# Performance work log

Measured on AMD Instinct MI355X. Metric: run time of the kernel, lower is better.

Reference implementation:

```python
import jax, jax.numpy as jnp
import numpy as np

B, S, D, H = 4, 1024, 1024, 16
DK = D // H
N_REL = 5


def setup_inputs() -> dict:
    key = jax.random.key(0)
    ks = jax.random.split(key, 16)
    p = lambda k, shape: (jax.random.normal(k, shape, dtype=jnp.float32) * 0.02)
    return {
        "x": jax.random.normal(ks[0], (B, S, D), dtype=jnp.float32),
        "relation_matrix": jax.random.randint(ks[1], (S, S), 0, N_REL, dtype=jnp.int32),
        "mask": jax.random.randint(ks[2], (B, 1, S, S), 0, 2, dtype=jnp.int32),
        "Wq": p(ks[3], (D, D)), "bq": p(ks[4], (D,)),
        "Wk": p(ks[5], (D, D)), "bk": p(ks[6], (D,)),
        "Wv": p(ks[7], (D, D)), "bv": p(ks[8], (D,)),
        "Wo": p(ks[9], (D, D)), "bo": p(ks[10], (D,)),
        "rel_table": p(ks[11], (N_REL, DK)),
        "gamma": jnp.ones((D,), dtype=jnp.float32),
        "beta": jnp.zeros((D,), dtype=jnp.float32),
    }


def reference(x, relation_matrix, mask, Wq, bq, Wk, bk, Wv, bv, Wo, bo, rel_table, gamma, beta):
    b, s = x.shape[0], x.shape[1]
    residual = x
    # projections -> [B, H, S, DK]
    def proj(W, bias):
        return (x @ W + bias).reshape(b, s, H, DK).transpose(0, 2, 1, 3)
    Q, K, V = proj(Wq, bq), proj(Wk, bk), proj(Wv, bv)
    scores = jnp.einsum('bhid,bhjd->bhij', Q, K) / jnp.sqrt(jnp.float32(DK))
    # relation-embedding additive bias: gather [S,S,DK] then contract with Q
    rel_emb = rel_table[relation_matrix]               # [S, S, DK]
    rel_scores = jnp.einsum('bhid,ijd->bhij', Q, rel_emb)
    scores = scores + rel_scores * 0.5
    scores = jnp.where(mask == 0, jnp.float32(-1e9), scores)
    attention = jax.nn.softmax(scores, axis=-1)
    context = jnp.einsum('bhij,bhjd->bhid', attention, V)
    context = context.transpose(0, 2, 1, 3).reshape(b, s, D)
    output = context @ Wo + bo
    # layer norm (eps = 1e-5, torch default)
    y = output + residual
    mu = jnp.mean(y, axis=-1, keepdims=True)
    var = jnp.mean(jnp.square(y - mu), axis=-1, keepdims=True)
    return (y - mu) * jax.lax.rsqrt(var + 1e-5) * gamma + beta
```

## Files before the change

kernel.cpp:

```cpp
#include <hip/hip_runtime.h>
#include <hip/hip_bf16.h>

typedef unsigned short u16;
typedef unsigned int u32;
typedef unsigned char u8;
typedef __attribute__((ext_vector_type(8))) short short8;
typedef __attribute__((ext_vector_type(4))) float f32x4;

__device__ __forceinline__ float b2f(u16 u) {
    union { float f; u32 i; } z; z.i = ((u32)u) << 16; return z.f;
}
__device__ __forceinline__ u16 f2b(float f) {
    union { float f; u32 i; } z; z.f = f;
    u32 i = z.i;
    u32 r = (i + 0x7FFFu + ((i >> 16) & 1u)) >> 16;
    return (u16)r;
}
__device__ __forceinline__ float ldf(const void* p, size_t i, int f) {
    return f ? ((const float*)p)[i] : b2f(((const u16*)p)[i]);
}
__device__ __forceinline__ void gload_lds16(const void* g, void* l) {
    __builtin_amdgcn_global_load_lds(
        (const __attribute__((address_space(1))) u32*)g,
        (__attribute__((address_space(3))) u32*)l,
        16, 0, 0);
}

struct P14 { const void* p[14]; };
struct S14 { int s[14]; };

__global__ __launch_bounds__(256) void classify(P14 ptrs, S14 szs, int* cls)
{
    __shared__ int   wsm[4], wzr[4], wag[4], way[4], wjk[4];
    __shared__ float wme[4], wmo[4];
    __shared__ int small_[14], zero_[14], gone_[14], junk_[14];
    __shared__ float maxe_[14], maxo_[14];
    int t = threadIdx.x, lane = t & 63, w = t >> 6;
    for (int i = 0; i < 14; ++i) {
        const u16* p16 = (const u16*)ptrs.p[i];
        const u32* p32 = (const u32*)ptrs.p[i];
        int n = szs.s[i];
        int n16 = n < 4096 ? n : 4096;
        int n32 = n16 >> 1;
        int small = 1, zero = 1, allg = 1, anyg = 0, junk = 0;
        float maxe = 0.f, maxo = 0.f;
        for (int k = t; k < n32; k += 256) if (p32[k] >= 8u) small = 0;
        for (int k = t; k < n16; k += 256) {
            u16 ww = p16[k];
            if (ww != 0) zero = 0;
            if (ww == 0x3F80u) anyg = 1;
            else if (ww != 0) allg = 0;
            float a = fabsf(b2f(ww));
            if (k & 1) { if (a < 1e30f && a > maxo) maxo = a; }
            else { if (!(a < 100.0f)) junk++; else if (a > maxe) maxe = a; }
        }
#pragma unroll
        for (int s = 1; s < 64; s <<= 1) {
            small &= __shfl_xor(small, s);
            zero  &= __shfl_xor(zero, s);
            allg  &= __shfl_xor(allg, s);
            anyg  |= __shfl_xor(anyg, s);
            junk  += __shfl_xor(junk, s);
            maxe   = fmaxf(maxe, __shfl_xor(maxe, s));
            maxo   = fmaxf(maxo, __shfl_xor(maxo, s));
        }
        if (lane == 0) { wsm[w]=small; wzr[w]=zero; wag[w]=allg; way[w]=anyg; wjk[w]=junk; wme[w]=maxe; wmo[w]=maxo; }
        __syncthreads();
        if (t == 0) {
            int sm=1,zr=1,ag=1,ay=0,jk=0; float me=0.f,mo=0.f;
            for (int q=0;q<4;++q){ sm&=wsm[q]; zr&=wzr[q]; ag&=wag[q]; ay|=way[q]; jk+=wjk[q]; me=fmaxf(me,wme[q]); mo=fmaxf(mo,wmo[q]); }
            small_[i]=sm; zero_[i]=zr; gone_[i]=ag&&ay; junk_[i]=jk; maxe_[i]=me; maxo_[i]=mo;
        }
        __syncthreads();
    }
    if (t == 0) {
        int xi = -1, mi = -1, ri = -1, rt = -1, gi = -1, bi = -1;
        int wv[4] = {-1,-1,-1,-1}; int nw = 0;
        int bs[4] = {-1,-1,-1,-1}; int nb = 0;
        for (int i = 0; i < 14; ++i) {
            int s = szs.s[i];
            if (s == 4194304) { if (small_[i]) mi = i; else xi = i; }
            else if (s == 1048576) { if (small_[i]) ri = i; else if (nw < 4) wv[nw++] = i; }
            else if (s == 320) rt = i;
            else if (s == 1024) {
                if (zero_[i]) bi = i;
                else if (gone_[i]) gi = i;
                else if (nb < 4) bs[nb++] = i;
            }
        }
        bool ok = (xi >= 0) && (mi >= 0) && (ri >= 0) && (rt >= 0) && (gi >= 0) && (bi >= 0)
               && (nw == 4) && (nb == 4);
        if (ok) {
            cls[0] = xi; cls[1] = ri; cls[2] = mi;
            cls[3] = wv[0]; cls[5] = wv[1]; cls[7] = wv[2]; cls[9] = wv[3];
            cls[4] = bs[0]; cls[6] = bs[1]; cls[8] = bs[2]; cls[10] = bs[3];
            cls[11] = rt; cls[12] = gi; cls[13] = bi;
        } else {
            for (int r = 0; r < 14; ++r) cls[r] = r;
        }
        const int froles[12] = {0,3,4,5,6,7,8,9,10,11,12,13};
        for (int r = 0; r < 12; ++r) {
            int role = froles[r]; int idx = cls[role];
            cls[16 + role] = (junk_[idx] > 0) || (maxe_[idx] == 0.f && maxo_[idx] > 0.f);
        }
        cls[30] = ok ? 1 : 0;
    }
}

__global__ __launch_bounds__(256) void cvt_x_flex(P14 ptrs, const int* cls, u16* xb) {
    const void* x = ptrs.p[cls[0]];
    int f = cls[16];
    int idx = (blockIdx.x * 256 + threadIdx.x) << 2;
    union { u16 u[4]; uint2 v2; } o;
    if (f) {
        float4 v = *(const float4*)((const float*)x + idx);
        o.u[0] = f2b(v.x); o.u[1] = f2b(v.y); o.u[2] = f2b(v.z); o.u[3] = f2b(v.w);
    } else {
        o.v2 = *(const uint2*)((const u16*)x + idx);
    }
    *(uint2*)&xb[idx] = o.v2;
}

__global__ __launch_bounds__(256) void transposeW_flex(P14 ptrs, const int* cls,
                                                       u16* WT3, u16* WoT)
{
    int z = blockIdx.z;
    const void* W = ptrs.p[cls[3 + 2 * z]];
    int f = cls[16 + 3 + 2 * z];
    u16* WT = (z < 3) ? (WT3 + ((size_t)z << 20)) : WoT;
    __shared__ u16 tile[64][72];
    int t = threadIdx.x;
    int n0 = blockIdx.x << 6, k0 = blockIdx.y << 6;
    int r = t >> 2, c = (t & 3) << 4;
    size_t base = (size_t)(k0 + r) * 1024 + n0 + c;
    if (f) {
        const float* src = (const float*)W + base;
#pragma unroll
        for (int x = 0; x < 16; ++x) tile[r][c + x] = f2b(src[x]);
    } else {
        const u16* src = (const u16*)W + base;
#pragma unroll
        for (int x = 0; x < 16; ++x) tile[r][c + x] = src[x];
    }
    __syncthreads();
    union { u16 u[16]; uint4 v[2]; } tmp;
#pragma unroll
    for (int x = 0; x < 16; ++x) tmp.u[x] = tile[c + x][r];
    *(uint4*)&WT[(size_t)(n0 + r) * 1024 + k0 + c]     = tmp.v[0];
    *(uint4*)&WT[(size_t)(n0 + r) * 1024 + k0 + c + 8] = tmp.v[1];
}

__global__ __launch_bounds__(256) void transposeV(const u16* __restrict__ Vb,
                                                  u16* __restrict__ VT)
{
    __shared__ u16 tile[64][72];
    int bh = blockIdx.y, j0 = blockIdx.x << 6;
    const u16* src = Vb + ((size_t)bh << 16);
    u16* dst = VT + ((size_t)bh << 16);
    int t = threadIdx.x, r = t >> 2, c = (t & 3) << 4;
    const u16* s = src + (size_t)(j0 + r) * 64 + c;
    *(uint4*)&tile[r][c]     = *(const uint4*)s;
    *(uint4*)&tile[r][c + 8] = *(const uint4*)(s + 8);
    __syncthreads();
    union { u16 u[16]; uint4 v[2]; } tmp;
#pragma unroll
    for (int x = 0; x < 16; ++x) tmp.u[x] = tile[c + x][r];
    u16* d = dst + (size_t)r * 1024 + j0 + c;
    *(uint4*)d       = tmp.v[0];
    *(uint4*)(d + 8) = tmp.v[1];
}

__global__ __launch_bounds__(256) void qrel_k(
    const u16* __restrict__ Q, P14 ptrs, const int* cls, float* __restrict__ Qrel)
{
    __shared__ float rt[5][64];
    const void* rel_table = ptrs.p[cls[11]];
    int f9 = cls[16 + 11];
    int t = threadIdx.x;
    for (int p = t; p < 320; p += 256) ((float*)rt)[p] = ldf(rel_table, p, f9);
    __syncthreads();
    int row = blockIdx.x * 256 + t;
    const u16* qrow = Q + ((size_t)row << 6);
    float a0=0.f, a1=0.f, a2=0.f, a3=0.f, a4=0.f;
#pragma unroll
    for (int k8 = 0; k8 < 64; k8 += 8) {
        union { uint4 v; u16 u[8]; } qq;
        qq.v = *(const uint4*)(qrow + k8);
#pragma unroll
        for (int e = 0; e < 8; ++e) {
            float qv = b2f(qq.u[e]);
            a0 += qv * rt[0][k8 + e];
            a1 += qv * rt[1][k8 + e];
            a2 += qv * rt[2][k8 + e];
            a3 += qv * rt[3][k8 + e];
            a4 += qv * rt[4][k8 + e];
        }
    }
    const float S = 0.5f * 1.44269504f;
    float4 o0 = {a0 * S, a1 * S, a2 * S, a3 * S};
    float4 o1 = {a4 * S, -1e9f, -1e9f, -1e9f};
    *(float4*)&Qrel[(size_t)row * 8]     = o0;
    *(float4*)&Qrel[(size_t)row * 8 + 4] = o1;
}

__global__ __launch_bounds__(256) void gemm128_qkv(
    const u16* __restrict__ X, const u16* __restrict__ WT3,
    P14 ptrs, const int* cls,
    u16* __restrict__ Qb, u16* __restrict__ Kb, u16* __restrict__ Vb)
{
    int z = blockIdx.z;
    const u16* WT = WT3 + ((size_t)z << 20);
    const void* biasp = ptrs.p[cls[4 + 2 * z]];
    int fb = cls[16 + 4 + 2 * z];
    u16* outp = (z == 0) ? Qb : (z == 1) ? Kb : Vb;
    int n0 = blockIdx.x << 7, m0 = blockIdx.y << 7;
    __shared__ u16 As[2][128][4][8];
    __shared__ u16 Bs[2][128][4][8];
    int t = threadIdx.x, lane = t & 63, w = t >> 6;
    int m = lane & 15, quad = lane >> 4;
    int wm = (w >> 1) << 6, wn = (w & 1) << 6;
    int r1 = t >> 2, r2 = 64 + r1, k4 = t & 3;
    const u16* xa  = &X [(size_t)(m0 + r1) * 1024 + k4 * 8];
    const u16* xa2 = &X [(size_t)(m0 + r2) * 1024 + k4 * 8];
    const u16* wb  = &WT[(size_t)(n0 + r1) * 1024 + k4 * 8];
    const u16* wb2 = &WT[(size_t)(n0 + r2) * 1024 + k4 * 8];
    f32x4 acc[4][4];
#pragma unroll
    for (int i = 0; i < 4; ++i)
#pragma unroll
        for (int j = 0; j < 4; ++j) acc[i][j] = (f32x4){0.f,0.f,0.f,0.f};

    auto stage = [&](int buf, int k0) {
        gload_lds16(xa  + k0, &As[buf][r1][k4][0]);
        gload_lds16(xa2 + k0, &As[buf][r2][k4][0]);
        gload_lds16(wb  + k0, &Bs[buf][r1][k4][0]);
        gload_lds16(wb2 + k0, &Bs[buf][r2][k4][0]);
    };
    stage(0, 0);
    __syncthreads();
    int cur = 0;
    for (int k0 = 0; k0 < 1024; k0 += 32) {
        if (k0 + 32 < 1024) stage(cur ^ 1, k0 + 32);
        short8 af[4], bf[4];
#pragma unroll
        for (int mb = 0; mb < 4; ++mb) af[mb] = *(const short8*)&As[cur][wm + mb*16 + m][quad][0];
#pragma unroll
        for (int nb = 0; nb < 4; ++nb) bf[nb] = *(const short8*)&Bs[cur][wn + nb*16 + m][quad][0];
#pragma unroll
        for (int mb = 0; mb < 4; ++mb)
#pragma unroll
            for (int nb = 0; nb < 4; ++nb)
                acc[mb][nb] = __builtin_amdgcn_mfma_f32_16x16x32_bf16(af[mb], bf[nb], acc[mb][nb], 0, 0, 0);
        __syncthreads();
        cur ^= 1;
    }
#pragma unroll
    for (int nb = 0; nb < 4; ++nb) {
        int gn = n0 + wn + nb*16 + m;
        int h = gn >> 6, dk = gn & 63;
        float bb = ldf(biasp, gn, fb);
#pragma unroll
        for (int mb = 0; mb < 4; ++mb)
#pragma unroll
            for (int r = 0; r < 4; ++r) {
                int gm = m0 + wm + mb*16 + (quad << 2) + r;
                int b = gm >> 10, s = gm & 1023;
                outp[((size_t)((b * 16 + h) << 10) + s) * 64 + dk] = f2b(acc[mb][nb][r] + bb);
            }
    }
}

__global__ __launch_bounds__(256) void gemm128_out(
    const u16* __restrict__ A, const u16* __restrict__ WT,
    P14 ptrs, const int* cls, float* __restrict__ y)
{
    const void* bo   = ptrs.p[cls[10]];
    const void* Xres = ptrs.p[cls[0]];
    int f8 = cls[16 + 10], f0 = cls[16];
    int n0 = blockIdx.x << 7, m0 = blockIdx.y << 7;
    __shared__ u16 As[2][128][4][8];
    __shared__ u16 Bs[2][128][4][8];
    int t = threadIdx.x, lane = t & 63, w = t >> 6;
    int m = lane & 15, quad = lane >> 4;
    int wm = (w >> 1) << 6, wn = (w & 1) << 6;
    int r1 = t >> 2, r2 = 64 + r1, k4 = t & 3;
    const u16* xa  = &A [(size_t)(m0 + r1) * 1024 + k4 * 8];
    const u16* xa2 = &A [(size_t)(m0 + r2) * 1024 + k4 * 8];
    const u16* wb  = &WT[(size_t)(n0 + r1) * 1024 + k4 * 8];
    const u16* wb2 = &WT[(size_t)(n0 + r2) * 1024 + k4 * 8];
    f32x4 acc[4][4];
#pragma unroll
    for (int i = 0; i < 4; ++i)
#pragma unroll
        for (int j = 0; j < 4; ++j) acc[i][j] = (f32x4){0.f,0.f,0.f,0.f};

    auto stage = [&](int buf, int k0) {
        gload_lds16(xa  + k0, &As[buf][r1][k4][0]);
        gload_lds16(xa2 + k0, &As[buf][r2][k4][0]);
        gload_lds16(wb  + k0, &Bs[buf][r1][k4][0]);
        gload_lds16(wb2 + k0, &Bs[buf][r2][k4][0]);
    };
    stage(0, 0);
    __syncthreads();
    int cur = 0;
    for (int k0 = 0; k0 < 1024; k0 += 32) {
        if (k0 + 32 < 1024) stage(cur ^ 1, k0 + 32);
        short8 af[4], bf[4];
#pragma unroll
        for (int mb = 0; mb < 4; ++mb) af[mb] = *(const short8*)&As[cur][wm + mb*16 + m][quad][0];
#pragma unroll
        for (int nb = 0; nb < 4; ++nb) bf[nb] = *(const short8*)&Bs[cur][wn + nb*16 + m][quad][0];
#pragma unroll
        for (int mb = 0; mb < 4; ++mb)
#pragma unroll
            for (int nb = 0; nb < 4; ++nb)
                acc[mb][nb] = __builtin_amdgcn_mfma_f32_16x16x32_bf16(af[mb], bf[nb], acc[mb][nb], 0, 0, 0);
        __syncthreads();
        cur ^= 1;
    }
#pragma unroll
    for (int nb = 0; nb < 4; ++nb) {
        int gn = n0 + wn + nb*16 + m;
        float bb = ldf(bo, gn, f8);
#pragma unroll
        for (int mb = 0; mb < 4; ++mb)
#pragma unroll
            for (int r = 0; r < 4; ++r) {
                int gm = m0 + wm + mb*16 + (quad << 2) + r;
                size_t idx = (size_t)gm * 1024 + gn;
                y[idx] = acc[mb][nb][r] + bb + ldf(Xres, idx, f0);
            }
    }
}

__global__ __launch_bounds__(256) void make_codes(P14 ptrs, const int* cls, u8* codes)
{
    const int* relmat = (const int*)ptrs.p[cls[1]];
    const int* maskp  = (const int*)ptrs.p[cls[2]];
    int bid = blockIdx.x;
    int b = bid >> 8, ti = (bid >> 4) & 15, tj = bid & 15;
    int t = threadIdx.x, lane = t & 63, w = t >> 6;
    int m = lane & 15, quad = lane >> 4;
    const int* mb = maskp + ((size_t)b << 20);
    union { uint4 v; u8 c[16]; } out;
#pragma unroll
    for (int jb = 0; jb < 4; ++jb) {
        int j = tj * 64 + jb * 16 + m;
#pragma unroll
        for (int r = 0; r < 4; ++r) {
            int i = ti * 64 + w * 16 + (quad << 2) + r;
            size_t off = (size_t)i * 1024 + j;
            out.c[jb * 4 + r] = mb[off] ? (u8)relmat[off] : (u8)5;
        }
    }
    ((uint4*)codes)[(size_t)bid * 256 + t] = out.v;
}

__global__ __launch_bounds__(256) void attn_mfma(
    const u16* __restrict__ Q, const u16* __restrict__ K, const u16* __restrict__ VT,
    const float* __restrict__ Qrel, const u8* __restrict__ codes, u16* __restrict__ ctx)
{
    int raw = blockIdx.x;
    int bid = (raw & 7) * 128 + (raw >> 3);
    int bh = bid >> 4, ti = bid & 15;
    int i0 = ti << 6;
    int b = bh >> 4, h = bh & 15;
    const u16* Qp = Q  + ((size_t)bh << 16);
    const u16* Kp = K  + ((size_t)bh << 16);
    const u16* Vp = VT + ((size_t)bh << 16);
    const uint4* ctile = (const uint4*)codes + ((size_t)((b * 16 + ti) * 16) << 8);

    __shared__ u16 Ks[64][72];
    __shared__ u16 Vt[64][72];
    __shared__ u16 Pls[64][72];
    __shared__ float Qrl[64][9];

    int t = threadIdx.x, lane = t & 63, w = t >> 6;
    int m = lane & 15, quad = lane >> 4;

    {
        float2 qv = *(const float2*)&Qrel[(((size_t)bh << 10) + i0) * 8 + (t << 1)];
        Qrl[t >> 2][(t & 3) << 1]       = qv.x;
        Qrl[t >> 2][((t & 3) << 1) + 1] = qv.y;
    }

    short8 qfrag0, qfrag1;
    {
        const u16* qr = Qp + (size_t)(i0 + w * 16 + m) * 64 + quad * 8;
        qfrag0 = *(const short8*)qr;
        qfrag1 = *(const short8*)(qr + 32);
    }
    f32x4 O[4];
    float l_part[4];
#pragma unroll
    for (int d = 0; d < 4; ++d) O[d] = (f32x4){0.f,0.f,0.f,0.f};
#pragma unroll
    for (int r = 0; r < 4; ++r) l_part[r] = 0.f;

    int srow = t >> 2, scol = (t & 3) << 4;
    const float SC = 0.125f * 1.44269504f;

    uint4 kA, kB, vA, vB, cN;
    auto issue = [&](int j0) {
        const u16* kr = Kp + (size_t)(j0 + srow) * 64 + scol;
        kA = *(const uint4*)kr;
        kB = *(const uint4*)(kr + 8);
        const u16* vr = Vp + (size_t)srow * 1024 + j0 + scol;
        vA = *(const uint4*)vr;
        vB = *(const uint4*)(vr + 8);
        cN = ctile[((j0 >> 6) << 8) + t];
    };
    issue(0);

    for (int j0 = 0; j0 < 1024; j0 += 64) {
        __syncthreads();
        *(uint4*)&Ks[srow][scol]     = kA;
        *(uint4*)&Ks[srow][scol + 8] = kB;
        *(uint4*)&Vt[srow][scol]     = vA;
        *(uint4*)&Vt[srow][scol + 8] = vB;
        union { uint4 v; u8 c[16]; } cd;
        cd.v = cN;
        __syncthreads();
        if (j0 + 64 < 1024) issue(j0 + 64);

        f32x4 acc[4];
#pragma unroll
        for (int jb = 0; jb < 4; ++jb) {
            acc[jb] = (f32x4){0.f,0.f,0.f,0.f};
            short8 kb0 = *(const short8*)&Ks[jb * 16 + m][quad * 8];
            short8 kb1 = *(const short8*)&Ks[jb * 16 + m][quad * 8 + 32];
            acc[jb] = __builtin_amdgcn_mfma_f32_16x16x32_bf16(qfrag0, kb0, acc[jb], 0, 0, 0);
            acc[jb] = __builtin_amdgcn_mfma_f32_16x16x32_bf16(qfrag1, kb1, acc[jb], 0, 0, 0);
        }
        float sc[4][4];
#pragma unroll
        for (int jb = 0; jb < 4; ++jb) {
#pragma unroll
            for (int r = 0; r < 4; ++r) {
                int il = w * 16 + (quad << 2) + r;
                float p = exp2f(acc[jb][r] * SC + Qrl[il][cd.c[jb * 4 + r]]);
                sc[jb][r] = p;
                l_part[r] += p;
            }
        }
#pragma unroll
        for (int jb = 0; jb < 4; ++jb)
#pragma unroll
            for (int r = 0; r < 4; ++r)
                Pls[w * 16 + (quad << 2) + r][jb * 16 + m] = f2b(sc[jb][r]);
        short8 pa0 = *(const short8*)&Pls[w * 16 + m][quad * 8];
        short8 pa1 = *(const short8*)&Pls[w * 16 + m][quad * 8 + 32];
#pragma unroll
        for (int db = 0; db < 4; ++db) {
            short8 vb0 = *(const short8*)&Vt[db * 16 + m][quad * 8];
            short8 vb1 = *(const short8*)&Vt[db * 16 + m][quad * 8 + 32];
            O[db] = __builtin_amdgcn_mfma_f32_16x16x32_bf16(pa0, vb0, O[db], 0, 0, 0);
            O[db] = __builtin_amdgcn_mfma_f32_16x16x32_bf16(pa1, vb1, O[db], 0, 0, 0);
        }
    }
    float linv[4];
#pragma unroll
    for (int r = 0; r < 4; ++r) {
        float l = l_part[r];
        l += __shfl_xor(l, 1);
        l += __shfl_xor(l, 2);
        l += __shfl_xor(l, 4);
        l += __shfl_xor(l, 8);
        linv[r] = 1.0f / fmaxf(l, 1e-35f);
    }
#pragma unroll
    for (int db = 0; db < 4; ++db)
#pragma unroll
        for (int r = 0; r < 4; ++r) {
            int il = w * 16 + (quad << 2) + r;
            size_t addr = ((size_t)(b * 1024 + i0 + il)) * 1024 + h * 64 + db * 16 + m;
            ctx[addr] = f2b(O[db][r] * linv[r]);
        }
}

__global__ __launch_bounds__(256) void ln_k(
    float* __restrict__ y, P14 ptrs, const int* cls)
{
    const void* gamma = ptrs.p[cls[12]];
    const void* beta  = ptrs.p[cls[13]];
    int f10 = cls[16 + 12], f11 = cls[16 + 13];
    int row = blockIdx.x, t = threadIdx.x;
    float4 v = *(const float4*)&y[(size_t)row * 1024 + (t << 2)];
    float s = v.x + v.y + v.z + v.w;
#pragma unroll
    for (int mm = 1; mm < 64; mm <<= 1) s += __shfl_xor(s, mm);
    __shared__ float sm[8];
    int w = t >> 6, lane = t & 63;
    if (lane == 0) sm[w] = s;
    __syncthreads();
    float mu = (sm[0] + sm[1] + sm[2] + sm[3]) * (1.0f / 1024.0f);
    float dx = v.x - mu, dy = v.y - mu, dz = v.z - mu, dw = v.w - mu;
    float q = dx * dx + dy * dy + dz * dz + dw * dw;
#pragma unroll
    for (int mm = 1; mm < 64; mm <<= 1) q += __shfl_xor(q, mm);
    if (lane == 0) sm[4 + w] = q;
    __syncthreads();
    float var = (sm[4] + sm[5] + sm[6] + sm[7]) * (1.0f / 1024.0f);
    float rs = rsqrtf(var + 1e-5f);
    int c = t << 2;
    float4 o;
    o.x = dx * rs * ldf(gamma, c,     f10) + ldf(beta, c,     f11);
    o.y = dy * rs * ldf(gamma, c + 1, f10) + ldf(beta, c + 1, f11);
    o.z = dz * rs * ldf(gamma, c + 2, f10) + ldf(beta, c + 2, f11);
    o.w = dw * rs * ldf(gamma, c + 3, f10) + ldf(beta, c + 3, f11);
    *(float4*)&y[(size_t)row * 1024 + c] = o;
}

extern "C" void kernel_launch(void* const* d_in, const int* in_sizes, int n_in,
                              void* d_out, int out_size, void* d_ws, size_t ws_size,
                              hipStream_t stream) {
    (void)out_size; (void)ws_size;
    P14 ptrs; S14 szs;
    for (int i = 0; i < 14; ++i) {
        ptrs.p[i] = (i < n_in) ? d_in[i] : d_in[0];
        szs.s[i]  = (i < n_in) ? in_sizes[i] : 0;
    }
    float* out = (float*)d_out;

    char* ws = (char*)d_ws;
    const size_t MB = 1u << 20;
    u16*   WT3   = (u16*)(ws);
    u16*   WoT   = (u16*)(ws + 6 * MB);
    u16*   Xb    = (u16*)(ws + 8 * MB);
    u16*   VbT   = (u16*)(ws + 8 * MB);
    u16*   Qb    = (u16*)(ws + 16 * MB);
    u16*   Kb    = (u16*)(ws + 24 * MB);
    u16*   Vb    = (u16*)(ws + 32 * MB);
    u16*   ctx   = (u16*)(ws + 32 * MB);
    u8*    codes = (u8*)(ws);
    float* Qrel  = (float*)(ws + 4 * MB);
    int*   cls   = (int*)(ws + 40 * MB);

    classify<<<1, 256, 0, stream>>>(ptrs, szs, cls);
    cvt_x_flex<<<4096, 256, 0, stream>>>(ptrs, cls, Xb);
    transposeW_flex<<<dim3(16, 16, 4), 256, 0, stream>>>(ptrs, cls, WT3, WoT);
    gemm128_qkv<<<dim3(8, 32, 3), 256, 0, stream>>>(Xb, WT3, ptrs, cls, Qb, Kb, Vb);
    transposeV<<<dim3(16, 64), 256, 0, stream>>>(Vb, VbT);
    qrel_k<<<256, 256, 0, stream>>>(Qb, ptrs, cls, Qrel);
    make_codes<<<1024, 256, 0, stream>>>(ptrs, cls, codes);
    attn_mfma<<<1024, 256, 0, stream>>>(Qb, Kb, VbT, Qrel, codes, ctx);
    gemm128_out<<<dim3(8, 32), 256, 0, stream>>>(ctx, WoT, ptrs, cls, out);
    ln_k<<<4096, 256, 0, stream>>>(out, ptrs, cls);
}
```

Before: 323.7 us.

## Double-buffer attention K/V tiles via direct-to-LDS loads with XOR swizzle; parallelize classify

The attention kernel now stages K and V tiles straight into double-buffered LDS with global_load_lds, replacing register staging and removing one barrier per iteration. K (in the QKV GEMM epilogue) and V^T (in the transpose) are written pre-swizzled in global memory so the unpadded 64-wide LDS tiles can be read with an XOR pattern that avoids bank conflicts. The single-block input classifier is split into a 14-block stats kernel plus a tiny bind kernel, which shortens a serial prologue at the cost of one extra launch. The swizzle has to agree exactly across three kernels, which adds correctness risk.

```diff
diff --git a/kernel.cpp b/kernel.cpp
--- a/kernel.cpp
+++ b/kernel.cpp
@@ -29,82 +29,85 @@
 struct P14 { const void* p[14]; };
 struct S14 { int s[14]; };
 
-__global__ __launch_bounds__(256) void classify(P14 ptrs, S14 szs, int* cls)
+__global__ __launch_bounds__(256) void classify_stats(P14 ptrs, S14 szs, int* stats)
 {
     __shared__ int   wsm[4], wzr[4], wag[4], way[4], wjk[4];
     __shared__ float wme[4], wmo[4];
-    __shared__ int small_[14], zero_[14], gone_[14], junk_[14];
-    __shared__ float maxe_[14], maxo_[14];
+    int i = blockIdx.x;
     int t = threadIdx.x, lane = t & 63, w = t >> 6;
+    const u16* p16 = (const u16*)ptrs.p[i];
+    const u32* p32 = (const u32*)ptrs.p[i];
+    int n = szs.s[i];
+    int n16 = n < 4096 ? n : 4096;
+    int n32 = n16 >> 1;
+    int small = 1, zero = 1, allg = 1, anyg = 0, junk = 0;
+    float maxe = 0.f, maxo = 0.f;
+    for (int k = t; k < n32; k += 256) if (p32[k] >= 8u) small = 0;
+    for (int k = t; k < n16; k += 256) {
+        u16 ww = p16[k];
+        if (ww != 0) zero = 0;
+        if (ww == 0x3F80u) anyg = 1;
+        else if (ww != 0) allg = 0;
+        float a = fabsf(b2f(ww));
+        if (k & 1) { if (a < 1e30f && a > maxo) maxo = a; }
+        else { if (!(a < 100.0f)) junk++; else if (a > maxe) maxe = a; }
+    }
+#pragma unroll
+    for (int s = 1; s < 64; s <<= 1) {
+        small &= __shfl_xor(small, s);
+        zero  &= __shfl_xor(zero, s);
+        allg  &= __shfl_xor(allg, s);
+        anyg  |= __shfl_xor(anyg, s);
+        junk  += __shfl_xor(junk, s);
+        maxe   = fmaxf(maxe, __shfl_xor(maxe, s));
+        maxo   = fmaxf(maxo, __shfl_xor(maxo, s));
+    }
+    if (lane == 0) { wsm[w]=small; wzr[w]=zero; wag[w]=allg; way[w]=anyg; wjk[w]=junk; wme[w]=maxe; wmo[w]=maxo; }
+    __syncthreads();
+    if (t == 0) {
+        int sm=1,zr=1,ag=1,ay=0,jk=0; float me=0.f,mo=0.f;
+        for (int q=0;q<4;++q){ sm&=wsm[q]; zr&=wzr[q]; ag&=wag[q]; ay|=way[q]; jk+=wjk[q]; me=fmaxf(me,wme[q]); mo=fmaxf(mo,wmo[q]); }
+        stats[i*8+0]=sm; stats[i*8+1]=zr; stats[i*8+2]=(ag&&ay)?1:0; stats[i*8+3]=jk;
+        stats[i*8+4]=__float_as_int(me); stats[i*8+5]=__float_as_int(mo);
+    }
+}
+
+__global__ __launch_bounds__(64) void classify_bind(S14 szs, const int* stats, int* cls)
+{
+    if (threadIdx.x != 0) return;
+    int xi = -1, mi = -1, ri = -1, rt = -1, gi = -1, bi = -1;
+    int wv[4] = {-1,-1,-1,-1}; int nw = 0;
+    int bs[4] = {-1,-1,-1,-1}; int nb = 0;
     for (int i = 0; i < 14; ++i) {
-        const u16* p16 = (const u16*)ptrs.p[i];
-        const u32* p32 = (const u32*)ptrs.p[i];
-        int n = szs.s[i];
-        int n16 = n < 4096 ? n : 4096;
-        int n32 = n16 >> 1;
-        int small = 1, zero = 1, allg = 1, anyg = 0, junk = 0;
-        float maxe = 0.f, maxo = 0.f;
-        for (int k = t; k < n32; k += 256) if (p32[k] >= 8u) small = 0;
-        for (int k = t; k < n16; k += 256) {
-            u16 ww = p16[k];
-            if (ww != 0) zero = 0;
-            if (ww == 0x3F80u) anyg = 1;
-            else if (ww != 0) allg = 0;
-            float a = fabsf(b2f(ww));
-            if (k & 1) { if (a < 1e30f && a > maxo) maxo = a; }
-            else { if (!(a < 100.0f)) junk++; else if (a > maxe) maxe = a; }
-        }
-#pragma unroll
-        for (int s = 1; s < 64; s <<= 1) {
-            small &= __shfl_xor(small, s);
-            zero  &= __shfl_xor(zero, s);
-            allg  &= __shfl_xor(allg, s);
-            anyg  |= __shfl_xor(anyg, s);
-            junk  += __shfl_xor(junk, s);
-            maxe   = fmaxf(maxe, __shfl_xor(maxe, s));
-            maxo   = fmaxf(maxo, __shfl_xor(maxo, s));
-        }
-        if (lane == 0) { wsm[w]=small; wzr[w]=zero; wag[w]=allg; way[w]=anyg; wjk[w]=junk; wme[w]=maxe; wmo[w]=maxo; }
-        __syncthreads();
-        if (t == 0) {
-            int sm=1,zr=1,ag=1,ay=0,jk=0; float me=0.f,mo=0.f;
-            for (int q=0;q<4;++q){ sm&=wsm[q]; zr&=wzr[q]; ag&=wag[q]; ay|=way[q]; jk+=wjk[q]; me=fmaxf(me,wme[q]); mo=fmaxf(mo,wmo[q]); }
-            small_[i]=sm; zero_[i]=zr; gone_[i]=ag&&ay; junk_[i]=jk; maxe_[i]=me; maxo_[i]=mo;
-        }
-        __syncthreads();
-    }
-    if (t == 0) {
-        int xi = -1, mi = -1, ri = -1, rt = -1, gi = -1, bi = -1;
-        int wv[4] = {-1,-1,-1,-1}; int nw = 0;
-        int bs[4] = {-1,-1,-1,-1}; int nb = 0;
-        for (int i = 0; i < 14; ++i) {
-            int s = szs.s[i];
-            if (s == 4194304) { if (small_[i]) mi = i; else xi = i; }
-            else if (s == 1048576) { if (small_[i]) ri = i; else if (nw < 4) wv[nw++] = i; }
-            else if (s == 320) rt = i;
-            else if (s == 1024) {
-                if (zero_[i]) bi = i;
-                else if (gone_[i]) gi = i;
-                else if (nb < 4) bs[nb++] = i;
-            }
-        }
-        bool ok = (xi >= 0) && (mi >= 0) && (ri >= 0) && (rt >= 0) && (gi >= 0) && (bi >= 0)
-               && (nw == 4) && (nb == 4);
-        if (ok) {
-            cls[0] = xi; cls[1] = ri; cls[2] = mi;
-            cls[3] = wv[0]; cls[5] = wv[1]; cls[7] = wv[2]; cls[9] = wv[3];
-            cls[4] = bs[0]; cls[6] = bs[1]; cls[8] = bs[2]; cls[10] = bs[3];
-            cls[11] = rt; cls[12] = gi; cls[13] = bi;
-        } else {
-            for (int r = 0; r < 14; ++r) cls[r] = r;
-        }
-        const int froles[12] = {0,3,4,5,6,7,8,9,10,11,12,13};
-        for (int r = 0; r < 12; ++r) {
-            int role = froles[r]; int idx = cls[role];
-            cls[16 + role] = (junk_[idx] > 0) || (maxe_[idx] == 0.f && maxo_[idx] > 0.f);
-        }
-        cls[30] = ok ? 1 : 0;
-    }
+        int s = szs.s[i];
+        int sm = stats[i*8+0], zr = stats[i*8+1];
+        if (s == 4194304) { if (sm) mi = i; else xi = i; }
+        else if (s == 1048576) { if (sm) ri = i; else if (nw < 4) wv[nw++] = i; }
+        else if (s == 320) rt = i;
+        else if (s == 1024) {
+            if (zr) bi = i;
+            else if (stats[i*8+2]) gi = i;
+            else if (nb < 4) bs[nb++] = i;
+        }
+    }
+    bool ok = (xi >= 0) && (mi >= 0) && (ri >= 0) && (rt >= 0) && (gi >= 0) && (bi >= 0)
+           && (nw == 4) && (nb == 4);
+    if (ok) {
+        cls[0] = xi; cls[1] = ri; cls[2] = mi;
+        cls[3] = wv[0]; cls[5] = wv[1]; cls[7] = wv[2]; cls[9] = wv[3];
+        cls[4] = bs[0]; cls[6] = bs[1]; cls[8] = bs[2]; cls[10] = bs[3];
+        cls[11] = rt; cls[12] = gi; cls[13] = bi;
+    } else {
+        for (int r = 0; r < 14; ++r) cls[r] = r;
+    }
+    const int froles[12] = {0,3,4,5,6,7,8,9,10,11,12,13};
+    for (int r = 0; r < 12; ++r) {
+        int role = froles[r]; int idx = cls[role];
+        float me = __int_as_float(stats[idx*8+4]);
+        float mo = __int_as_float(stats[idx*8+5]);
+        cls[16 + role] = (stats[idx*8+3] > 0) || (me == 0.f && mo > 0.f);
+    }
+    cls[30] = ok ? 1 : 0;
 }
 
 __global__ __launch_bounds__(256) void cvt_x_flex(P14 ptrs, const int* cls, u16* xb) {
@@ -165,9 +168,12 @@
     union { u16 u[16]; uint4 v[2]; } tmp;
 #pragma unroll
     for (int x = 0; x < 16; ++x) tmp.u[x] = tile[c + x][r];
-    u16* d = dst + (size_t)r * 1024 + j0 + c;
-    *(uint4*)d       = tmp.v[0];
-    *(uint4*)(d + 8) = tmp.v[1];
+    int swz = (r & 7) << 3;
+    int c2 = c ^ (swz & 48);
+    int hsw = (swz >> 3) & 1;
+    u16* d = dst + (size_t)r * 1024 + j0 + c2;
+    *(uint4*)d       = tmp.v[hsw];
+    *(uint4*)(d + 8) = tmp.v[1 - hsw];
 }
 
 __global__ __launch_bounds__(256) void qrel_k(
@@ -265,7 +271,8 @@
             for (int r = 0; r < 4; ++r) {
                 int gm = m0 + wm + mb*16 + (quad << 2) + r;
                 int b = gm >> 10, s = gm & 1023;
-                outp[((size_t)((b * 16 + h) << 10) + s) * 64 + dk] = f2b(acc[mb][nb][r] + bb);
+                int dk2 = (z == 1) ? (dk ^ (((quad * 4 + r) & 7) << 3)) : dk;
+                outp[((size_t)((b * 16 + h) << 10) + s) * 64 + dk2] = f2b(acc[mb][nb][r] + bb);
             }
     }
 }
@@ -370,8 +377,8 @@
     const u16* Vp = VT + ((size_t)bh << 16);
     const uint4* ctile = (const uint4*)codes + ((size_t)((b * 16 + ti) * 16) << 8);
 
-    __shared__ u16 Ks[64][72];
-    __shared__ u16 Vt[64][72];
+    __shared__ u16 Ks[2][64][64];
+    __shared__ u16 Vt[2][64][64];
     __shared__ u16 Pls[64][72];
     __shared__ float Qrl[64][9];
 
@@ -397,38 +404,39 @@
 #pragma unroll
     for (int r = 0; r < 4; ++r) l_part[r] = 0.f;
 
-    int srow = t >> 2, scol = (t & 3) << 4;
+    int srow = t >> 3, scol8 = (t & 7) << 3;
+    const u16* ks0 = Kp + (size_t)srow * 64 + scol8;
+    const u16* ks1 = ks0 + 32 * 64;
+    const u16* vs0 = Vp + (size_t)srow * 1024 + scol8;
+    const u16* vs1 = vs0 + 32 * 1024;
+
+    auto stage = [&](int buf, int j0) {
+        gload_lds16(ks0 + (size_t)j0 * 64, &Ks[buf][srow][scol8]);
+        gload_lds16(ks1 + (size_t)j0 * 64, &Ks[buf][srow + 32][scol8]);
+        gload_lds16(vs0 + j0, &Vt[buf][srow][scol8]);
+        gload_lds16(vs1 + j0, &Vt[buf][srow + 32][scol8]);
+    };
+
     const float SC = 0.125f * 1.44269504f;
-
-    uint4 kA, kB, vA, vB, cN;
-    auto issue = [&](int j0) {
-        const u16* kr = Kp + (size_t)(j0 + srow) * 64 + scol;
-        kA = *(const uint4*)kr;
-        kB = *(const uint4*)(kr + 8);
-        const u16* vr = Vp + (size_t)srow * 1024 + j0 + scol;
-        vA = *(const uint4*)vr;
-        vB = *(const uint4*)(vr + 8);
-        cN = ctile[((j0 >> 6) << 8) + t];
-    };
-    issue(0);
+    int kx = (m & 7) << 3;
+
+    stage(0, 0);
+    uint4 cN = ctile[t];
+    __syncthreads();
+    int cur = 0;
 
     for (int j0 = 0; j0 < 1024; j0 += 64) {
-        __syncthreads();
-        *(uint4*)&Ks[srow][scol]     = kA;
-        *(uint4*)&Ks[srow][scol + 8] = kB;
-        *(uint4*)&Vt[srow][scol]     = vA;
-        *(uint4*)&Vt[srow][scol + 8] = vB;
+        if (j0 + 64 < 1024) stage(cur ^ 1, j0 + 64);
         union { uint4 v; u8 c[16]; } cd;
         cd.v = cN;
-        __syncthreads();
-        if (j0 + 64 < 1024) issue(j0 + 64);
+        if (j0 + 64 < 1024) cN = ctile[(((j0 + 64) >> 6) << 8) + t];
 
         f32x4 acc[4];
 #pragma unroll
         for (int jb = 0; jb < 4; ++jb) {
             acc[jb] = (f32x4){0.f,0.f,0.f,0.f};
-            short8 kb0 = *(const short8*)&Ks[jb * 16 + m][quad * 8];
-            short8 kb1 = *(const short8*)&Ks[jb * 16 + m][quad * 8 + 32];
+            short8 kb0 = *(const short8*)&Ks[cur][jb * 16 + m][(quad * 8) ^ kx];
+            short8 kb1 = *(const short8*)&Ks[cur][jb * 16 + m][(32 + quad * 8) ^ kx];
             acc[jb] = __builtin_amdgcn_mfma_f32_16x16x32_bf16(qfrag0, kb0, acc[jb], 0, 0, 0);
             acc[jb] = __builtin_amdgcn_mfma_f32_16x16x32_bf16(qfrag1, kb1, acc[jb], 0, 0, 0);
         }
@@ -452,11 +460,13 @@
         short8 pa1 = *(const short8*)&Pls[w * 16 + m][quad * 8 + 32];
 #pragma unroll
         for (int db = 0; db < 4; ++db) {
-            short8 vb0 = *(const short8*)&Vt[db * 16 + m][quad * 8];
-            short8 vb1 = *(const short8*)&Vt[db * 16 + m][quad * 8 + 32];
+            short8 vb0 = *(const short8*)&Vt[cur][db * 16 + m][(quad * 8) ^ kx];
+            short8 vb1 = *(const short8*)&Vt[cur][db * 16 + m][(32 + quad * 8) ^ kx];
             O[db] = __builtin_amdgcn_mfma_f32_16x16x32_bf16(pa0, vb0, O[db], 0, 0, 0);
             O[db] = __builtin_amdgcn_mfma_f32_16x16x32_bf16(pa1, vb1, O[db], 0, 0, 0);
         }
+        __syncthreads();
+        cur ^= 1;
     }
     float linv[4];
 #pragma unroll
@@ -535,8 +545,10 @@
     u8*    codes = (u8*)(ws);
     float* Qrel  = (float*)(ws + 4 * MB);
     int*   cls   = (int*)(ws + 40 * MB);
-
-    classify<<<1, 256, 0, stream>>>(ptrs, szs, cls);
+    int*   stats = (int*)(ws + 40 * MB + 512);
+
+    classify_stats<<<14, 256, 0, stream>>>(ptrs, szs, stats);
+    classify_bind<<<1, 64, 0, stream>>>(szs, stats, cls);
     cvt_x_flex<<<4096, 256, 0, stream>>>(ptrs, cls, Xb);
     transposeW_flex<<<dim3(16, 16, 4), 256, 0, stream>>>(ptrs, cls, WT3, WoT);
     gemm128_qkv<<<dim3(8, 32, 3), 256, 0, stream>>>(Xb, WT3, ptrs, cls, Qb, Kb, Vb);
```

Result: faster. 301.2 us (-6.9%).
